# Optimization experiments

Hardware: AMD Instinct MI355X
Metric: run time of the kernel (lower is better)

The kernel has to match this reference:

```python
import jax, jax.numpy as jnp
import numpy as np

EPS = 1e-10


def setup_inputs() -> dict:
    key = jax.random.key(0)
    k1, k2 = jax.random.split(key)
    x = jax.random.normal(k1, (8, 16, 512, 512), dtype=jnp.float32)
    # inv_grid in [-1, 1], grid_sample-style normalized coordinates
    inv_grid = jax.random.uniform(k2, (8, 512, 512, 2), dtype=jnp.float32,
                                  minval=-1.0, maxval=1.0)
    return {"x": x, "inv_grid": inv_grid}


def reference(x, inv_grid):
    bs, nc, h, w = x.shape  # OH=OW=None -> output spatial dims = input dims
    g = (inv_grid + 1.0) * 0.5
    # map to padded pixel coords and clamp, exactly as the torch module
    gi = jnp.clip(g[..., 0] * h + 1.0, 0.0, h + 1 - 2 * EPS).reshape(-1)
    gj = jnp.clip(g[..., 1] * w + 1.0, 0.0, w + 1 - 2 * EPS).reshape(-1)
    ii = gi.astype(jnp.int32)  # floor (coords are non-negative)
    jj = gj.astype(jnp.int32)
    npix = inv_grid.shape[1] * inv_grid.shape[2]
    b_idx = jnp.repeat(jnp.arange(bs, dtype=jnp.int32), npix)
    H3, W3 = h + 3, w + 3
    Bflat = jnp.zeros((bs * H3 * W3,), dtype=jnp.float32)
    # 4-corner bilinear splat scatter-add; denominator is channel-independent
    for di in (0, 1):
        wi = jax.nn.relu(1.0 - jnp.abs(gi - (ii + di).astype(gi.dtype)))
        for dj in (0, 1):
            wj = jax.nn.relu(1.0 - jnp.abs(gj - (jj + dj).astype(gj.dtype)))
            idx = (b_idx * H3 + (ii + di)) * W3 + (jj + dj)
            Bflat = Bflat.at[idx].add(wi * wj)
    Bden = Bflat.reshape(bs, H3, W3)[:, 1:h + 1, 1:w + 1]
    # torch adds the same B_ch to every channel -> broadcast over C
    return jnp.broadcast_to(Bden[:, None], (bs, nc, h, w))
```

## Files before the change

kernel.cpp:

```cpp
#include <hip/hip_runtime.h>

#define BS 8
#define NC 16
#define H 512
#define W 512
#define RB 17
#define NKH 62
#define CHUNKS 1024
#define CHPB 128
#define CPTS 2048
#define CAP 3072
#define ACC_ROWS 19
#define ACC_W 264
#define ACC_ELEMS (ACC_ROWS * ACC_W)
#define GRID2 (BS * NKH)
#define FIX_SCALE 16777216.0f
#define FIX_INV   5.9604644775390625e-8f

typedef float f32x4 __attribute__((ext_vector_type(4)));

__global__ __launch_bounds__(512)
void k1_bin(const float* __restrict__ inv_grid,
            float2* __restrict__ bins,
            unsigned* __restrict__ chunkOff) {
    __shared__ float2 stage[CAP];
    __shared__ unsigned cnt[NKH];
    __shared__ unsigned off[64];
    const int blk = blockIdx.x, tid = threadIdx.x;
    if (tid < NKH) cnt[tid] = 0;
    __syncthreads();

    const float4* src = reinterpret_cast<const float4*>(inv_grid)
                      + (size_t)blk * (CPTS / 2);
    float2 pg[4];
    unsigned dk[4][4];
#pragma unroll
    for (int i = 0; i < 2; ++i) {
        float4 v = src[tid + i * 512];
#pragma unroll
        for (int s = 0; s < 2; ++s) {
            const int p = i * 2 + s;
            float gx = s ? v.z : v.x;
            float gy = s ? v.w : v.y;
            float gi = fminf(fmaxf((gx + 1.0f) * 0.5f * (float)H + 1.0f, 0.0f), 513.0f);
            float gj = fminf(fmaxf((gy + 1.0f) * 0.5f * (float)W + 1.0f, 0.0f), 513.0f);
            int ii = (int)gi, jj = (int)gj;
            int k = ii / RB;
            bool rd = (ii - k * RB == RB - 1);
            int h = (jj >= 256) ? 1 : 0;
            bool cd = (jj == 256);
            pg[p] = make_float2(gi, gj);
            unsigned bk0 = (unsigned)(2 * k + h);
            dk[p][0] = (bk0 << 13) | atomicAdd(&cnt[bk0], 1u);
            dk[p][1] = dk[p][2] = dk[p][3] = 0xFFFFFFFFu;
            if (rd) { unsigned b1 = bk0 + 2;
                      dk[p][1] = (b1 << 13) | atomicAdd(&cnt[b1], 1u); }
            if (cd) { unsigned b2 = (unsigned)(2 * k);
                      dk[p][2] = (b2 << 13) | atomicAdd(&cnt[b2], 1u);
                if (rd) { unsigned b3 = b2 + 2;
                          dk[p][3] = (b3 << 13) | atomicAdd(&cnt[b3], 1u); } }
        }
    }
    __syncthreads();
    if (tid < 64) {
        unsigned v = (tid < NKH) ? cnt[tid] : 0u;
#pragma unroll
        for (int d = 1; d < 64; d <<= 1) {
            unsigned o = __shfl_up(v, d, 64);
            if (tid >= d) v += o;
        }
        if (tid == 0) off[0] = 0u;
        if (tid < 63) off[tid + 1] = v;
    }
    __syncthreads();
    if (tid < 63) chunkOff[blk * 64 + tid] = off[tid];
#pragma unroll
    for (int p = 0; p < 4; ++p)
#pragma unroll
        for (int q = 0; q < 4; ++q) {
            unsigned d = dk[p][q];
            if (d != 0xFFFFFFFFu) {
                unsigned pos = off[d >> 13] + (d & 8191u);
                if (pos < CAP) stage[pos] = pg[p];
            }
        }
    __syncthreads();
    unsigned total = off[62];
    if (total > CAP) total = CAP;
    float2* dst = bins + (size_t)blk * CAP;
    for (unsigned i = tid; i < total; i += 512) dst[i] = stage[i];
}

__global__ __launch_bounds__(1024)
void k2_splat_store(const float2* __restrict__ bins,
                    const unsigned* __restrict__ chunkOff,
                    float* __restrict__ out) {
    __shared__ unsigned acc[ACC_ELEMS];
    __shared__ unsigned segstart[CHPB], segn[CHPB];
    const int bucket = blockIdx.x;
    const int b = bucket / NKH;
    const int kh = bucket % NKH;
    const int k = kh >> 1, h = kh & 1;
    const int r0 = k * RB;
    const int col0 = 1 + (h << 8);
    const int tid = threadIdx.x;

    for (int i = tid; i < ACC_ELEMS; i += 1024) acc[i] = 0u;
    if (tid < CHPB) {
        const unsigned* row = chunkOff + (size_t)(b * CHPB + tid) * 64;
        unsigned s0 = row[kh], s1 = row[kh + 1];
        segstart[tid] = s0;
        segn[tid] = s1 - s0;
    }
    __syncthreads();

    const int g = tid >> 4, lane = tid & 15;
#pragma unroll
    for (int pass = 0; pass < 2; ++pass) {
        const int seg = g + pass * 64;
        const float2* base = bins + (size_t)(b * CHPB + seg) * CAP + segstart[seg];
        const unsigned n = segn[seg];
        for (unsigned idx = lane; idx < n; idx += 16) {
            float2 p = base[idx];
            int ii = (int)p.x, jj = (int)p.y;
            float fi = p.x - (float)ii, fj = p.y - (float)jj;
            float a = 1.0f - fi, c = 1.0f - fj;
            int ofs = (ii - r0 + 1) * ACC_W + (jj - col0 + 4);
            atomicAdd(&acc[ofs],             (unsigned)(a  * c  * FIX_SCALE + 0.5f));
            atomicAdd(&acc[ofs + 1],         (unsigned)(a  * fj * FIX_SCALE + 0.5f));
            atomicAdd(&acc[ofs + ACC_W],     (unsigned)(fi * c  * FIX_SCALE + 0.5f));
            atomicAdd(&acc[ofs + ACC_W + 1], (unsigned)(fi * fj * FIX_SCALE + 0.5f));
        }
    }
    __syncthreads();

    const int l = tid & 63, wv = tid >> 6;
    for (int it = wv; it < RB * NC; it += 16) {
        int d = it >> 4, c = it & 15;
        int r = r0 + d;
        if (r < 1 || r > H) continue;
        const unsigned* ap = acc + (d + 1) * ACC_W + 4 + 4 * l;
        uint4 q = *reinterpret_cast<const uint4*>(ap);
        f32x4 v;
        v.x = (float)q.x * FIX_INV; v.y = (float)q.y * FIX_INV;
        v.z = (float)q.z * FIX_INV; v.w = (float)q.w * FIX_INV;
        size_t o = (((size_t)(b * NC + c)) * H + (r - 1)) * (size_t)W
                 + (h << 8) + 4 * l;
        __builtin_nontemporal_store(v, reinterpret_cast<f32x4*>(out + o));
    }
}

extern "C" void kernel_launch(void* const* d_in, const int* in_sizes, int n_in,
                              void* d_out, int out_size, void* d_ws, size_t ws_size,
                              hipStream_t stream) {
    const float* inv_grid = (const float*)d_in[1];
    float* out = (float*)d_out;

    float2*   bins     = (float2*)d_ws;
    unsigned* chunkOff = (unsigned*)((char*)d_ws + (size_t)CHUNKS * CAP * sizeof(float2));

    k1_bin<<<CHUNKS, 512, 0, stream>>>(inv_grid, bins, chunkOff);
    k2_splat_store<<<GRID2, 1024, 0, stream>>>(bins, chunkOff, out);
}
```

Before: 45.69 us.

## Pack splat records into 32-bit and merge column halves per block

The binning kernel now stores each point as one packed 32-bit record: local row, a 9-bit row fraction, local column and a 9-bit column fraction. This replaces the float2 of absolute coordinates and halves the intermediate traffic. Duplicates routed to neighbouring buckets get their local indices fixed with constant offsets. The splat kernel processes both column halves of a row band in one block using two shared accumulators, so the block count halves and the store of the first half overlaps with the splat of the second. Quantizing the fractions to 1/512 adds error to the bilinear weights, which may exceed tolerance.

Result: faster. 44.67 us (-2.2%).

```diff
diff --git a/kernel.cpp b/kernel.cpp
--- a/kernel.cpp
+++ b/kernel.cpp
@@ -5,6 +5,7 @@
 #define H 512
 #define W 512
 #define RB 17
+#define TPB 31
 #define NKH 62
 #define CHUNKS 1024
 #define CHPB 128
@@ -13,17 +14,19 @@
 #define ACC_ROWS 19
 #define ACC_W 264
 #define ACC_ELEMS (ACC_ROWS * ACC_W)
-#define GRID2 (BS * NKH)
+#define GRID2 (BS * TPB)
 #define FIX_SCALE 16777216.0f
 #define FIX_INV   5.9604644775390625e-8f
+#define INV512    0.001953125f
 
 typedef float f32x4 __attribute__((ext_vector_type(4)));
 
+
 __global__ __launch_bounds__(512)
 void k1_bin(const float* __restrict__ inv_grid,
-            float2* __restrict__ bins,
+            unsigned* __restrict__ bins,
             unsigned* __restrict__ chunkOff) {
-    __shared__ float2 stage[CAP];
+    __shared__ unsigned stage[CAP];
     __shared__ unsigned cnt[NKH];
     __shared__ unsigned off[64];
     const int blk = blockIdx.x, tid = threadIdx.x;
@@ -32,7 +35,7 @@
 
     const float4* src = reinterpret_cast<const float4*>(inv_grid)
                       + (size_t)blk * (CPTS / 2);
-    float2 pg[4];
+    unsigned rec0[4];
     unsigned dk[4][4];
 #pragma unroll
     for (int i = 0; i < 2; ++i) {
@@ -49,16 +52,19 @@
             bool rd = (ii - k * RB == RB - 1);
             int h = (jj >= 256) ? 1 : 0;
             bool cd = (jj == 256);
-            pg[p] = make_float2(gi, gj);
+            unsigned fi9 = (unsigned)((gi - (float)ii) * 512.0f + 0.5f);
+            if (fi9 > 511u) fi9 = 511u;
+            unsigned fj9 = (unsigned)((gj - (float)jj) * 512.0f + 0.5f);
+            if (fj9 > 511u) fj9 = 511u;
+            unsigned il = (unsigned)(ii - k * RB + 1);
+            unsigned jl = (unsigned)(jj - (h << 8));
+            rec0[p] = (il << 27) | (fi9 << 18) | (jl << 9) | fj9;
             unsigned bk0 = (unsigned)(2 * k + h);
             dk[p][0] = (bk0 << 13) | atomicAdd(&cnt[bk0], 1u);
             dk[p][1] = dk[p][2] = dk[p][3] = 0xFFFFFFFFu;
-            if (rd) { unsigned b1 = bk0 + 2;
-                      dk[p][1] = (b1 << 13) | atomicAdd(&cnt[b1], 1u); }
-            if (cd) { unsigned b2 = (unsigned)(2 * k);
-                      dk[p][2] = (b2 << 13) | atomicAdd(&cnt[b2], 1u);
-                if (rd) { unsigned b3 = b2 + 2;
-                          dk[p][3] = (b3 << 13) | atomicAdd(&cnt[b3], 1u); } }
+            if (rd) dk[p][1] = ((bk0 + 2) << 13) | atomicAdd(&cnt[bk0 + 2], 1u);
+            if (cd) { dk[p][2] = ((bk0 - 1) << 13) | atomicAdd(&cnt[bk0 - 1], 1u);
+                if (rd) dk[p][3] = ((bk0 + 1) << 13) | atomicAdd(&cnt[bk0 + 1], 1u); }
         }
     }
     __syncthreads();
@@ -74,6 +80,11 @@
     }
     __syncthreads();
     if (tid < 63) chunkOff[blk * 64 + tid] = off[tid];
+    const unsigned ADJ0 = 0u;
+    const unsigned ADJ1 = 0u - (17u << 27);
+    const unsigned ADJ2 = (256u << 9);
+    const unsigned ADJ3 = ADJ1 + ADJ2;
+    const unsigned adj[4] = {ADJ0, ADJ1, ADJ2, ADJ3};
 #pragma unroll
     for (int p = 0; p < 4; ++p)
 #pragma unroll
@@ -81,59 +92,45 @@
             unsigned d = dk[p][q];
             if (d != 0xFFFFFFFFu) {
                 unsigned pos = off[d >> 13] + (d & 8191u);
-                if (pos < CAP) stage[pos] = pg[p];
+                if (pos < CAP) stage[pos] = rec0[p] + adj[q];
             }
         }
     __syncthreads();
     unsigned total = off[62];
     if (total > CAP) total = CAP;
-    float2* dst = bins + (size_t)blk * CAP;
-    for (unsigned i = tid; i < total; i += 512) dst[i] = stage[i];
+    unsigned* dst = bins + (size_t)blk * CAP;
+    for (unsigned i = tid; i < total; i += 512)
+        __builtin_nontemporal_store(stage[i], dst + i);
 }
 
-__global__ __launch_bounds__(1024)
-void k2_splat_store(const float2* __restrict__ bins,
-                    const unsigned* __restrict__ chunkOff,
-                    float* __restrict__ out) {
-    __shared__ unsigned acc[ACC_ELEMS];
-    __shared__ unsigned segstart[CHPB], segn[CHPB];
-    const int bucket = blockIdx.x;
-    const int b = bucket / NKH;
-    const int kh = bucket % NKH;
-    const int k = kh >> 1, h = kh & 1;
-    const int r0 = k * RB;
-    const int col0 = 1 + (h << 8);
-    const int tid = threadIdx.x;
-
-    for (int i = tid; i < ACC_ELEMS; i += 1024) acc[i] = 0u;
-    if (tid < CHPB) {
-        const unsigned* row = chunkOff + (size_t)(b * CHPB + tid) * 64;
-        unsigned s0 = row[kh], s1 = row[kh + 1];
-        segstart[tid] = s0;
-        segn[tid] = s1 - s0;
-    }
-    __syncthreads();
-
+__device__ __forceinline__ void splat_half(const unsigned* __restrict__ bins,
+                                           unsigned* acc,
+                                           const unsigned* segs, const unsigned* segn,
+                                           int bBase, int tid) {
     const int g = tid >> 4, lane = tid & 15;
 #pragma unroll
     for (int pass = 0; pass < 2; ++pass) {
         const int seg = g + pass * 64;
-        const float2* base = bins + (size_t)(b * CHPB + seg) * CAP + segstart[seg];
+        const unsigned* base = bins + (size_t)(bBase + seg) * CAP + segs[seg];
         const unsigned n = segn[seg];
         for (unsigned idx = lane; idx < n; idx += 16) {
-            float2 p = base[idx];
-            int ii = (int)p.x, jj = (int)p.y;
-            float fi = p.x - (float)ii, fj = p.y - (float)jj;
+            unsigned rec = base[idx];
+            unsigned il = rec >> 27;
+            float fi = (float)((rec >> 18) & 511u) * INV512;
+            unsigned jl = (rec >> 9) & 511u;
+            float fj = (float)(rec & 511u) * INV512;
             float a = 1.0f - fi, c = 1.0f - fj;
-            int ofs = (ii - r0 + 1) * ACC_W + (jj - col0 + 4);
+            unsigned ofs = il * ACC_W + jl + 3;
             atomicAdd(&acc[ofs],             (unsigned)(a  * c  * FIX_SCALE + 0.5f));
             atomicAdd(&acc[ofs + 1],         (unsigned)(a  * fj * FIX_SCALE + 0.5f));
             atomicAdd(&acc[ofs + ACC_W],     (unsigned)(fi * c  * FIX_SCALE + 0.5f));
             atomicAdd(&acc[ofs + ACC_W + 1], (unsigned)(fi * fj * FIX_SCALE + 0.5f));
         }
     }
-    __syncthreads();
+}
 
+__device__ __forceinline__ void store_half(const unsigned* acc, float* __restrict__ out,
+                                           int b, int r0, int h, int tid) {
     const int l = tid & 63, wv = tid >> 6;
     for (int it = wv; it < RB * NC; it += 16) {
         int d = it >> 4, c = it & 15;
@@ -150,14 +147,42 @@
     }
 }
 
+__global__ __launch_bounds__(1024)
+void k2_splat_store(const unsigned* __restrict__ bins,
+                    const unsigned* __restrict__ chunkOff,
+                    float* __restrict__ out) {
+    __shared__ unsigned accA[ACC_ELEMS], accB[ACC_ELEMS];
+    __shared__ unsigned sA[CHPB], nA[CHPB], sB[CHPB], nB[CHPB];
+    const int blk = blockIdx.x;
+    const int b = blk / TPB, k = blk % TPB;
+    const int r0 = k * RB;
+    const int tid = threadIdx.x;
+
+    for (int i = tid; i < ACC_ELEMS; i += 1024) { accA[i] = 0u; accB[i] = 0u; }
+    if (tid < CHPB) {
+        const unsigned* row = chunkOff + (size_t)(b * CHPB + tid) * 64;
+        unsigned x0 = row[2 * k], x1 = row[2 * k + 1], x2 = row[2 * k + 2];
+        sA[tid] = x0; nA[tid] = x1 - x0;
+        sB[tid] = x1; nB[tid] = x2 - x1;
+    }
+    __syncthreads();
+
+    splat_half(bins, accA, sA, nA, b * CHPB, tid);
+    __syncthreads();
+    store_half(accA, out, b, r0, 0, tid);
+    splat_half(bins, accB, sB, nB, b * CHPB, tid);
+    __syncthreads();
+    store_half(accB, out, b, r0, 1, tid);
+}
+
 extern "C" void kernel_launch(void* const* d_in, const int* in_sizes, int n_in,
                               void* d_out, int out_size, void* d_ws, size_t ws_size,
                               hipStream_t stream) {
     const float* inv_grid = (const float*)d_in[1];
     float* out = (float*)d_out;
 
-    float2*   bins     = (float2*)d_ws;
-    unsigned* chunkOff = (unsigned*)((char*)d_ws + (size_t)CHUNKS * CAP * sizeof(float2));
+    unsigned* bins     = (unsigned*)d_ws;
+    unsigned* chunkOff = (unsigned*)((char*)d_ws + (size_t)CHUNKS * CAP * sizeof(unsigned));
 
     k1_bin<<<CHUNKS, 512, 0, stream>>>(inv_grid, bins, chunkOff);
     k2_splat_store<<<GRID2, 1024, 0, stream>>>(bins, chunkOff, out);
```
